# Kernel tuning notes

Measured on AMD Instinct MI355X. Metric: run time of the kernel, lower is better.

The kernel has to match this reference:

```python
import jax, jax.numpy as jnp
import numpy as np

N = 50000
E = 800000
IN = 64
HID = 64
OUT = 32
R = 8
B = 8
EPS = 1e-5


def setup_inputs() -> dict:
    key = jax.random.key(0)
    ks = jax.random.split(key, 20)
    s_in = 1.0 / np.sqrt(IN)
    s_hid = 1.0 / np.sqrt(HID)
    inp = {
        "x": jax.random.normal(ks[0], (N, IN), dtype=jnp.float32),
        "edge_index": jax.random.randint(ks[1], (2, E), 0, N, dtype=jnp.int64) if jax.config.jax_enable_x64 else jax.random.randint(ks[1], (2, E), 0, N),
        "edge_type": jax.random.randint(ks[2], (E,), 0, R),
        # conv1: in -> hid
        "comp1": jax.random.normal(ks[3], (R, B), dtype=jnp.float32) * (1.0 / np.sqrt(B)),
        "bases1": jax.random.normal(ks[4], (B, IN, HID), dtype=jnp.float32) * s_in,
        "root1": jax.random.normal(ks[5], (IN, HID), dtype=jnp.float32) * s_in,
        "bias1": jnp.zeros((HID,), dtype=jnp.float32),
        # conv2 (hidden): hid -> hid
        "comp2": jax.random.normal(ks[6], (R, B), dtype=jnp.float32) * (1.0 / np.sqrt(B)),
        "bases2": jax.random.normal(ks[7], (B, HID, HID), dtype=jnp.float32) * s_hid,
        "root2": jax.random.normal(ks[8], (HID, HID), dtype=jnp.float32) * s_hid,
        "bias2": jnp.zeros((HID,), dtype=jnp.float32),
        # conv_out: hid -> out
        "comp3": jax.random.normal(ks[9], (R, B), dtype=jnp.float32) * (1.0 / np.sqrt(B)),
        "bases3": jax.random.normal(ks[10], (B, HID, OUT), dtype=jnp.float32) * s_hid,
        "root3": jax.random.normal(ks[11], (HID, OUT), dtype=jnp.float32) * s_hid,
        "bias3": jnp.zeros((OUT,), dtype=jnp.float32),
        # batchnorms
        "gamma1": jnp.ones((HID,), dtype=jnp.float32),
        "beta1": jnp.zeros((HID,), dtype=jnp.float32),
        "gamma2": jnp.ones((HID,), dtype=jnp.float32),
        "beta2": jnp.zeros((HID,), dtype=jnp.float32),
    }
    return inp


def rgcn_conv(x, src, dst, etype, comp, bases, root, bias):
    """PyG-style RGCNConv with basis decomposition and per-relation mean aggregation."""
    n = x.shape[0]
    # project node features through all bases: [N, B, O]
    xb = jnp.einsum('ni,bio->nbo', x, bases)
    # per-edge relation coefficients [E, B] contract with gathered basis features [E, B, O]
    msg = jnp.einsum('eb,ebo->eo', comp[etype], xb[src])
    # mean normalization per (dst node, relation)
    seg = dst * R + etype
    cnt = jax.ops.segment_sum(jnp.ones((msg.shape[0],), dtype=x.dtype), seg, num_segments=n * R)
    msg = msg / jnp.maximum(cnt[seg], 1.0)[:, None]
    agg = jax.ops.segment_sum(msg, dst, num_segments=n)
    return agg + x @ root + bias


def batch_norm(x, gamma, beta):
    mu = jnp.mean(x, axis=0)
    var = jnp.mean(jnp.square(x - mu), axis=0)  # biased, as torch BN training
    return (x - mu) * jax.lax.rsqrt(var + EPS) * gamma + beta


def reference(x, edge_index, edge_type, comp1, bases1, root1, bias1,
              comp2, bases2, root2, bias2, comp3, bases3, root3, bias3,
              gamma1, beta1, gamma2, beta2):
    src, dst = edge_index[0], edge_index[1]
    h = rgcn_conv(x, src, dst, edge_type, comp1, bases1, root1, bias1)
    h = batch_norm(jax.nn.relu(h), gamma1, beta1)  # dropout = identity (eval)
    h_res = h  # residual since in_channels == hidden_channels
    h2 = rgcn_conv(h, src, dst, edge_type, comp2, bases2, root2, bias2)
    h2 = batch_norm(jax.nn.relu(h2), gamma2, beta2)
    h = h2 + h_res
    out = rgcn_conv(h, src, dst, edge_type, comp3, bases3, root3, bias3)
    return out
```

## Files before the change

### kernel.cpp

```cpp
#include <hip/hip_runtime.h>

#define NN 50000
#define NE 800000
#define RR 8
#define BB 8
#define EPSV 1e-5f
#define SCAN_B ((NN + 255) / 256)
#define NGRP 64

typedef unsigned short bfu;
typedef signed char i8;
typedef __attribute__((ext_vector_type(8))) short bf16x8;
typedef __attribute__((ext_vector_type(4))) float f32x4;

__device__ inline float bf2f(bfu u) { return __uint_as_float(((unsigned)u) << 16); }
__device__ inline bfu f2bf(float f) {
    unsigned u = __float_as_uint(f);
    return (bfu)((u + 0x7fffu + ((u >> 16) & 1u)) >> 16);
}

#define NW1 36864L
#define NW2 36864L
#define NW3 18432L
#define NZ  (400000L + 50000L + 2L * NGRP * 128)

__device__ inline void build_one(const float* __restrict__ comp, const float* __restrict__ bases,
                                 const float* __restrict__ root, bfu* __restrict__ Wp,
                                 int O, int idx) {
    int k = idx / O, o = idx % O;
    float val;
    if (k < 512) {
        int r = k >> 6, i = k & 63;
        val = 0.f;
#pragma unroll
        for (int b = 0; b < BB; ++b)
            val += comp[r * BB + b] * bases[(b * 64 + i) * O + o];
    } else {
        val = root[(k - 512) * O + o];
    }
    int kt = k >> 5, kk = k & 31;
    int lane = ((kk >> 3) << 4) | (o & 15);
    int pos = ((kt * (O / 16) + (o >> 4)) * 64 + lane) * 8 + (kk & 7);
    Wp[pos] = f2bf(val);
}

__global__ void prep(const float* __restrict__ c1, const float* __restrict__ b1,
                     const float* __restrict__ r1, bfu* __restrict__ Wp1,
                     const float* __restrict__ c2, const float* __restrict__ b2,
                     const float* __restrict__ r2, bfu* __restrict__ Wp2,
                     const float* __restrict__ c3, const float* __restrict__ b3,
                     const float* __restrict__ r3, bfu* __restrict__ Wp3,
                     float* __restrict__ zbase) {
    long i = (long)blockIdx.x * blockDim.x + threadIdx.x;
    long stride = (long)gridDim.x * blockDim.x;
    const long tot = NW1 + NW2 + NW3 + NZ;
    for (; i < tot; i += stride) {
        if (i < NW1) build_one(c1, b1, r1, Wp1, 64, (int)i);
        else if (i < NW1 + NW2) build_one(c2, b2, r2, Wp2, 64, (int)(i - NW1));
        else if (i < NW1 + NW2 + NW3) build_one(c3, b3, r3, Wp3, 32, (int)(i - NW1 - NW2));
        else zbase[i - (NW1 + NW2 + NW3)] = 0.f;
    }
}

__global__ __launch_bounds__(256) void cvt_rows(const float* __restrict__ x,
                                                bfu* __restrict__ xb,
                                                i8* __restrict__ x8,
                                                float* __restrict__ xs) {
    int wv = threadIdx.x >> 6, lane = threadIdx.x & 63;
    int gw = blockIdx.x * 4 + wv, nw = gridDim.x * 4;
    for (int n = gw; n < NN; n += nw) {
        float v = x[(size_t)n * 64 + lane];
        xb[(size_t)n * 64 + lane] = f2bf(v);
        float am = fabsf(v);
#pragma unroll
        for (int d = 1; d < 64; d <<= 1) am = fmaxf(am, __shfl_xor(am, d));
        am = fmaxf(am, 1e-20f);
        float inv = 127.f / am;
        x8[(size_t)n * 64 + lane] = (i8)__float2int_rn(v * inv);
        if (lane == 0) xs[n] = am * (1.f / 127.f);
    }
}

__global__ void edge_count(const int* __restrict__ ei, const int* __restrict__ et,
                           float* __restrict__ cnt) {
    int range = blockIdx.x >> 8;
    int lo = range * (NN / 8), hi = lo + NN / 8;
    int i = (blockIdx.x & 255) * 256 + threadIdx.x;
    for (int e = i; e < NE; e += 256 * 256) {
        int d = ei[NE + e];
        if (d >= lo && d < hi)
            atomicAdd(&cnt[(size_t)d * RR + et[e]], 1.0f);
    }
}

__global__ void scan1(const float* __restrict__ cnt, int* __restrict__ offs, int* __restrict__ bsum) {
    __shared__ int sh[256];
    int b = blockIdx.x, t = threadIdx.x;
    int i = b * 256 + t;
    int v = 0;
    if (i < NN) {
        float s = 0.f;
#pragma unroll
        for (int r = 0; r < RR; ++r) s += cnt[(size_t)i * RR + r];
        v = (int)s;
    }
    sh[t] = v;
    __syncthreads();
    for (int s = 1; s < 256; s <<= 1) {
        int tmp = (t >= s) ? sh[t - s] : 0;
        __syncthreads();
        sh[t] += tmp;
        __syncthreads();
    }
    if (i < NN) offs[i] = sh[t] - v;
    if (t == 255) bsum[b] = sh[255];
}

__global__ void scan2(int* __restrict__ bsum, int* __restrict__ offs) {
    if (threadIdx.x == 0 && blockIdx.x == 0) {
        int run = 0;
        for (int b = 0; b < SCAN_B; ++b) { int t = bsum[b]; bsum[b] = run; run += t; }
        offs[NN] = run;
    }
}

__global__ void scan3(int* __restrict__ offs, const int* __restrict__ bsum) {
    int b = blockIdx.x, t = threadIdx.x;
    int i = b * 256 + t;
    if (i < NN) offs[i] += bsum[b];
}

__global__ void place(const int* __restrict__ ei, const int* __restrict__ et,
                      const int* __restrict__ offs, int* __restrict__ fill,
                      unsigned* __restrict__ esrt) {
    int range = blockIdx.x >> 8;
    int lo = range * (NN / 8), hi = lo + NN / 8;
    int i = (blockIdx.x & 255) * 256 + threadIdx.x;
    for (int e = i; e < NE; e += 256 * 256) {
        int d = ei[NE + e];
        if (d >= lo && d < hi) {
            int pos = offs[d] + atomicAdd(&fill[d], 1);
            esrt[pos] = ((unsigned)ei[e] << 3) | (unsigned)et[e];
        }
    }
}

#define ACCUMS(SU, V)                          \
    switch ((SU) & 7) {                        \
        case 0: a0 += (V); break;              \
        case 1: a1 += (V); break;              \
        case 2: a2 += (V); break;              \
        case 3: a3 += (V); break;              \
        case 4: a4 += (V); break;              \
        case 5: a5 += (V); break;              \
        case 6: a6 += (V); break;              \
        default: a7 += (V); break;             \
    }
#define RDL(X, L) __builtin_amdgcn_readlane((int)(X), (L))

template <int O, bool RELU, bool STATS>
__global__ __launch_bounds__(512, 8) void agg_gemm(const int* __restrict__ offs,
                                                   const unsigned* __restrict__ esrt,
                                                   const float* __restrict__ cnt,
                                                   const i8* __restrict__ x8,
                                                   const float* __restrict__ xs,
                                                   const bfu* __restrict__ xb,
                                                   const bfu* __restrict__ Wp,
                                                   const float* __restrict__ bias,
                                                   float* __restrict__ outp,
                                                   float* __restrict__ stats) {
    constexpr int CT = O / 16;
    __shared__ bfu Af[1152 * 8];
    int wave = threadIdx.x >> 6, lane = threadIdx.x & 63;
    int n0 = blockIdx.x * 16;
    int c = lane;
    int swz_lo = ((c >> 3) & 3) << 4;

#pragma unroll 1
    for (int i = 0; i < 2; ++i) {
        int row = wave * 2 + i;
        int n = n0 + row;
        int j0 = offs[n], j1 = offs[n + 1];
        float a0 = 0.f, a1 = 0.f, a2 = 0.f, a3 = 0.f, a4 = 0.f, a5 = 0.f, a6 = 0.f, a7 = 0.f;
        int j = j0;
        for (; j + 8 <= j1; j += 8) {
            unsigned mye = esrt[j + (lane & 7)];
            int s0 = RDL(mye, 0), s1 = RDL(mye, 1), s2 = RDL(mye, 2), s3 = RDL(mye, 3);
            int s4 = RDL(mye, 4), s5 = RDL(mye, 5), s6 = RDL(mye, 6), s7 = RDL(mye, 7);
            float q0 = (float)x8[(size_t)((unsigned)s0 >> 3) * 64 + lane];
            float q1 = (float)x8[(size_t)((unsigned)s1 >> 3) * 64 + lane];
            float q2 = (float)x8[(size_t)((unsigned)s2 >> 3) * 64 + lane];
            float q3 = (float)x8[(size_t)((unsigned)s3 >> 3) * 64 + lane];
            float q4 = (float)x8[(size_t)((unsigned)s4 >> 3) * 64 + lane];
            float q5 = (float)x8[(size_t)((unsigned)s5 >> 3) * 64 + lane];
            float q6 = (float)x8[(size_t)((unsigned)s6 >> 3) * 64 + lane];
            float q7 = (float)x8[(size_t)((unsigned)s7 >> 3) * 64 + lane];
            float c0 = xs[(unsigned)s0 >> 3], c1 = xs[(unsigned)s1 >> 3];
            float c2 = xs[(unsigned)s2 >> 3], c3 = xs[(unsigned)s3 >> 3];
            float c4 = xs[(unsigned)s4 >> 3], c5 = xs[(unsigned)s5 >> 3];
            float c6 = xs[(unsigned)s6 >> 3], c7 = xs[(unsigned)s7 >> 3];
            ACCUMS(s0, q0 * c0) ACCUMS(s1, q1 * c1) ACCUMS(s2, q2 * c2) ACCUMS(s3, q3 * c3)
            ACCUMS(s4, q4 * c4) ACCUMS(s5, q5 * c5) ACCUMS(s6, q6 * c6) ACCUMS(s7, q7 * c7)
        }
        if (j + 4 <= j1) {
            unsigned mye = esrt[j + (lane & 3)];
            int s0 = RDL(mye, 0), s1 = RDL(mye, 1), s2 = RDL(mye, 2), s3 = RDL(mye, 3);
            float q0 = (float)x8[(size_t)((unsigned)s0 >> 3) * 64 + lane];
            float q1 = (float)x8[(size_t)((unsigned)s1 >> 3) * 64 + lane];
            float q2 = (float)x8[(size_t)((unsigned)s2 >> 3) * 64 + lane];
            float q3 = (float)x8[(size_t)((unsigned)s3 >> 3) * 64 + lane];
            float c0 = xs[(unsigned)s0 >> 3], c1 = xs[(unsigned)s1 >> 3];
            float c2 = xs[(unsigned)s2 >> 3], c3 = xs[(unsigned)s3 >> 3];
            ACCUMS(s0, q0 * c0) ACCUMS(s1, q1 * c1) ACCUMS(s2, q2 * c2) ACCUMS(s3, q3 * c3)
            j += 4;
        }
        for (; j < j1; ++j) {
            int s0 = __builtin_amdgcn_readfirstlane((int)esrt[j]);
            float q0 = (float)x8[(size_t)((unsigned)s0 >> 3) * 64 + lane];
            float c0 = xs[(unsigned)s0 >> 3];
            ACCUMS(s0, q0 * c0)
        }
#define WR(r, ar) {                                                            \
        float inv = 1.f / fmaxf(cnt[(size_t)n * RR + (r)], 1.f);               \
        bfu bv = f2bf((ar) * inv);                                             \
        int g = (2 * (r) + (c >> 5)) * 64 + (row | swz_lo);                    \
        int gs = g ^ ((g >> 3) & 7) ^ ((g >> 6) & 7);                          \
        Af[gs * 8 + (c & 7)] = bv; }
        WR(0, a0) WR(1, a1) WR(2, a2) WR(3, a3)
        WR(4, a4) WR(5, a5) WR(6, a6) WR(7, a7)
#undef WR
        {
            bfu bv = xb[(size_t)n * 64 + lane];
            int g = (16 + (c >> 5)) * 64 + (row | swz_lo);
            int gs = g ^ ((g >> 3) & 7) ^ ((g >> 6) & 7);
            Af[gs * 8 + (c & 7)] = bv;
        }
    }
    __syncthreads();

    int ct = wave;
    if (ct < CT) {
        f32x4 acc = (f32x4){0.f, 0.f, 0.f, 0.f};
#pragma unroll
        for (int kt = 0; kt < 18; ++kt) {
            int g = kt * 64 + lane;
            int gs = g ^ ((g >> 3) & 7) ^ ((g >> 6) & 7);
            bf16x8 af = *(const bf16x8*)&Af[gs * 8];
            bf16x8 bfv = *(const bf16x8*)&Wp[((size_t)(kt * CT + ct) * 64 + lane) * 8];
            acc = __builtin_amdgcn_mfma_f32_16x16x32_bf16(af, bfv, acc, 0, 0, 0);
        }
        int col = ct * 16 + (lane & 15);
        float b = bias[col];
        float ssum = 0.f, sq = 0.f;
#pragma unroll
        for (int jj = 0; jj < 4; ++jj) {
            int row = (lane >> 4) * 4 + jj;
            float v = acc[jj] + b;
            if (RELU) v = fmaxf(v, 0.f);
            outp[(size_t)(n0 + row) * O + col] = v;
            if (STATS) { ssum += v; sq += v * v; }
        }
        if (STATS) {
            ssum += __shfl_xor(ssum, 16); ssum += __shfl_xor(ssum, 32);
            sq   += __shfl_xor(sq, 16);   sq   += __shfl_xor(sq, 32);
            if ((lane >> 4) == 0) {
                int g = blockIdx.x & (NGRP - 1);
                atomicAdd(&stats[g * 128 + col], ssum);
                atomicAdd(&stats[g * 128 + 64 + col], sq);
            }
        }
    }
}

template <bool HASRES>
__global__ __launch_bounds__(256) void bn_apply(const float* __restrict__ y,
                                                const float* __restrict__ stats,
                                                const float* __restrict__ gamma,
                                                const float* __restrict__ beta,
                                                const bfu* __restrict__ resb,
                                                bfu* __restrict__ hb,
                                                i8* __restrict__ h8,
                                                float* __restrict__ hs) {
    __shared__ float sc[128];
    int t = threadIdx.x;
    if (t < 64) {
        float s = 0.f, q = 0.f;
        for (int g = 0; g < NGRP; ++g) {
            s += stats[g * 128 + t];
            q += stats[g * 128 + 64 + t];
        }
        float mu = s / (float)NN;
        float var = q / (float)NN - mu * mu;
        float scale = gamma[t] * rsqrtf(var + EPSV);
        sc[t] = scale;
        sc[64 + t] = beta[t] - mu * scale;
    }
    __syncthreads();
    int wv = threadIdx.x >> 6, lane = threadIdx.x & 63;
    int gw = blockIdx.x * 4 + wv, nw = gridDim.x * 4;
    for (int n = gw; n < NN; n += nw) {
        float v = y[(size_t)n * 64 + lane] * sc[lane] + sc[64 + lane];
        if (HASRES) v += bf2f(resb[(size_t)n * 64 + lane]);
        hb[(size_t)n * 64 + lane] = f2bf(v);
        float am = fabsf(v);
#pragma unroll
        for (int d = 1; d < 64; d <<= 1) am = fmaxf(am, __shfl_xor(am, d));
        am = fmaxf(am, 1e-20f);
        float inv = 127.f / am;
        h8[(size_t)n * 64 + lane] = (i8)__float2int_rn(v * inv);
        if (lane == 0) hs[n] = am * (1.f / 127.f);
    }
}

extern "C" void kernel_launch(void* const* d_in, const int* in_sizes, int n_in,
                              void* d_out, int out_size, void* d_ws, size_t ws_size,
                              hipStream_t stream) {
    const float* x      = (const float*)d_in[0];
    const int*   ei     = (const int*)d_in[1];
    const int*   et     = (const int*)d_in[2];
    const float* comp1  = (const float*)d_in[3];
    const float* bases1 = (const float*)d_in[4];
    const float* root1  = (const float*)d_in[5];
    const float* bias1  = (const float*)d_in[6];
    const float* comp2  = (const float*)d_in[7];
    const float* bases2 = (const float*)d_in[8];
    const float* root2  = (const float*)d_in[9];
    const float* bias2  = (const float*)d_in[10];
    const float* comp3  = (const float*)d_in[11];
    const float* bases3 = (const float*)d_in[12];
    const float* root3  = (const float*)d_in[13];
    const float* bias3  = (const float*)d_in[14];
    const float* gamma1 = (const float*)d_in[15];
    const float* beta1  = (const float*)d_in[16];
    const float* gamma2 = (const float*)d_in[17];
    const float* beta2  = (const float*)d_in[18];
    float* out = (float*)d_out;

    float* ws = (float*)d_ws;
    size_t off = 0;
    bfu* Wp1 = (bfu*)(ws + off); off += 18432;
    bfu* Wp2 = (bfu*)(ws + off); off += 18432;
    bfu* Wp3 = (bfu*)(ws + off); off += 9216;
    float* cnt    = ws + off; off += (size_t)NN * RR;
    int*   fill   = (int*)(ws + off); off += NN;
    float* stats1 = ws + off; off += NGRP * 128;
    float* stats2 = ws + off; off += NGRP * 128;
    float* y  = ws + off; off += (size_t)NN * 64;
    bfu* xb   = (bfu*)(ws + off); off += (size_t)NN * 32;
    bfu* h1b  = (bfu*)(ws + off); off += (size_t)NN * 32;
    bfu* hb   = (bfu*)(ws + off); off += (size_t)NN * 32;
    i8*  x8   = (i8*)(ws + off);  off += (size_t)NN * 16;
    i8*  h1_8 = (i8*)(ws + off);  off += (size_t)NN * 16;
    i8*  h_8  = (i8*)(ws + off);  off += (size_t)NN * 16;
    float* xsc  = ws + off; off += NN;
    float* h1sc = ws + off; off += NN;
    float* hsc  = ws + off; off += NN;
    int* offs = (int*)(ws + off); off += NN + 4;
    int* bsum = (int*)(ws + off); off += 256;
    unsigned* esrt = (unsigned*)(ws + off); off += NE;

    prep<<<dim3(1024), dim3(256), 0, stream>>>(comp1, bases1, root1, Wp1,
                                               comp2, bases2, root2, Wp2,
                                               comp3, bases3, root3, Wp3, cnt);
    cvt_rows<<<dim3(512), dim3(256), 0, stream>>>(x, xb, x8, xsc);
    edge_count<<<dim3(2048), dim3(256), 0, stream>>>(ei, et, cnt);
    scan1<<<dim3(SCAN_B), dim3(256), 0, stream>>>(cnt, offs, bsum);
    scan2<<<dim3(1), dim3(64), 0, stream>>>(bsum, offs);
    scan3<<<dim3(SCAN_B), dim3(256), 0, stream>>>(offs, bsum);
    place<<<dim3(2048), dim3(256), 0, stream>>>(ei, et, offs, fill, esrt);

    agg_gemm<64, true, true><<<dim3(NN / 16), dim3(512), 0, stream>>>(offs, esrt, cnt, x8, xsc, xb, Wp1, bias1, y, stats1);
    bn_apply<false><<<dim3(1024), dim3(256), 0, stream>>>(y, stats1, gamma1, beta1, nullptr, h1b, h1_8, h1sc);

    agg_gemm<64, true, true><<<dim3(NN / 16), dim3(512), 0, stream>>>(offs, esrt, cnt, h1_8, h1sc, h1b, Wp2, bias2, y, stats2);
    bn_apply<true><<<dim3(1024), dim3(256), 0, stream>>>(y, stats2, gamma2, beta2, h1b, hb, h_8, hsc);

    agg_gemm<32, false, false><<<dim3(NN / 16), dim3(512), 0, stream>>>(offs, esrt, cnt, h_8, hsc, hb, Wp3, bias3, out, nullptr);
}
```

Baseline: 304.9 us.

## Use one row per wave, prefetch edge batches, and broadcast scales via readlane

agg_gemm now runs 16 waves per block, each handling one destination row instead of two in sequence, which exposes more parallel gather latency. The edge index batch for the next iteration is prefetched, and per-source scales are loaded once per lane and broadcast with readlane instead of eight scalar loads. edge_count and place now split the destination range into 4 partitions instead of 8, which halves their grids. The larger 1024-thread blocks may reduce occupancy flexibility, and with fewer partitions the atomics are less localized.

```diff
diff --git a/kernel.cpp b/kernel.cpp
--- a/kernel.cpp
+++ b/kernel.cpp
@@ -84,7 +84,7 @@
 __global__ void edge_count(const int* __restrict__ ei, const int* __restrict__ et,
                            float* __restrict__ cnt) {
     int range = blockIdx.x >> 8;
-    int lo = range * (NN / 8), hi = lo + NN / 8;
+    int lo = range * (NN / 4), hi = lo + NN / 4;
     int i = (blockIdx.x & 255) * 256 + threadIdx.x;
     for (int e = i; e < NE; e += 256 * 256) {
         int d = ei[NE + e];
@@ -134,7 +134,7 @@
                       const int* __restrict__ offs, int* __restrict__ fill,
                       unsigned* __restrict__ esrt) {
     int range = blockIdx.x >> 8;
-    int lo = range * (NN / 8), hi = lo + NN / 8;
+    int lo = range * (NN / 4), hi = lo + NN / 4;
     int i = (blockIdx.x & 255) * 256 + threadIdx.x;
     for (int e = i; e < NE; e += 256 * 256) {
         int d = ei[NE + e];
@@ -159,82 +159,88 @@
 #define RDL(X, L) __builtin_amdgcn_readlane((int)(X), (L))
 
 template <int O, bool RELU, bool STATS>
-__global__ __launch_bounds__(512, 8) void agg_gemm(const int* __restrict__ offs,
-                                                   const unsigned* __restrict__ esrt,
-                                                   const float* __restrict__ cnt,
-                                                   const i8* __restrict__ x8,
-                                                   const float* __restrict__ xs,
-                                                   const bfu* __restrict__ xb,
-                                                   const bfu* __restrict__ Wp,
-                                                   const float* __restrict__ bias,
-                                                   float* __restrict__ outp,
-                                                   float* __restrict__ stats) {
+__global__ __launch_bounds__(1024, 8) void agg_gemm(const int* __restrict__ offs,
+                                                    const unsigned* __restrict__ esrt,
+                                                    const float* __restrict__ cnt,
+                                                    const i8* __restrict__ x8,
+                                                    const float* __restrict__ xs,
+                                                    const bfu* __restrict__ xb,
+                                                    const bfu* __restrict__ Wp,
+                                                    const float* __restrict__ bias,
+                                                    float* __restrict__ outp,
+                                                    float* __restrict__ stats) {
     constexpr int CT = O / 16;
     __shared__ bfu Af[1152 * 8];
     int wave = threadIdx.x >> 6, lane = threadIdx.x & 63;
     int n0 = blockIdx.x * 16;
+    int row = wave;
+    int n = n0 + row;
     int c = lane;
     int swz_lo = ((c >> 3) & 3) << 4;
 
-#pragma unroll 1
-    for (int i = 0; i < 2; ++i) {
-        int row = wave * 2 + i;
-        int n = n0 + row;
-        int j0 = offs[n], j1 = offs[n + 1];
-        float a0 = 0.f, a1 = 0.f, a2 = 0.f, a3 = 0.f, a4 = 0.f, a5 = 0.f, a6 = 0.f, a7 = 0.f;
-        int j = j0;
-        for (; j + 8 <= j1; j += 8) {
-            unsigned mye = esrt[j + (lane & 7)];
-            int s0 = RDL(mye, 0), s1 = RDL(mye, 1), s2 = RDL(mye, 2), s3 = RDL(mye, 3);
-            int s4 = RDL(mye, 4), s5 = RDL(mye, 5), s6 = RDL(mye, 6), s7 = RDL(mye, 7);
-            float q0 = (float)x8[(size_t)((unsigned)s0 >> 3) * 64 + lane];
-            float q1 = (float)x8[(size_t)((unsigned)s1 >> 3) * 64 + lane];
-            float q2 = (float)x8[(size_t)((unsigned)s2 >> 3) * 64 + lane];
-            float q3 = (float)x8[(size_t)((unsigned)s3 >> 3) * 64 + lane];
-            float q4 = (float)x8[(size_t)((unsigned)s4 >> 3) * 64 + lane];
-            float q5 = (float)x8[(size_t)((unsigned)s5 >> 3) * 64 + lane];
-            float q6 = (float)x8[(size_t)((unsigned)s6 >> 3) * 64 + lane];
-            float q7 = (float)x8[(size_t)((unsigned)s7 >> 3) * 64 + lane];
-            float c0 = xs[(unsigned)s0 >> 3], c1 = xs[(unsigned)s1 >> 3];
-            float c2 = xs[(unsigned)s2 >> 3], c3 = xs[(unsigned)s3 >> 3];
-            float c4 = xs[(unsigned)s4 >> 3], c5 = xs[(unsigned)s5 >> 3];
-            float c6 = xs[(unsigned)s6 >> 3], c7 = xs[(unsigned)s7 >> 3];
-            ACCUMS(s0, q0 * c0) ACCUMS(s1, q1 * c1) ACCUMS(s2, q2 * c2) ACCUMS(s3, q3 * c3)
-            ACCUMS(s4, q4 * c4) ACCUMS(s5, q5 * c5) ACCUMS(s6, q6 * c6) ACCUMS(s7, q7 * c7)
-        }
-        if (j + 4 <= j1) {
-            unsigned mye = esrt[j + (lane & 3)];
-            int s0 = RDL(mye, 0), s1 = RDL(mye, 1), s2 = RDL(mye, 2), s3 = RDL(mye, 3);
-            float q0 = (float)x8[(size_t)((unsigned)s0 >> 3) * 64 + lane];
-            float q1 = (float)x8[(size_t)((unsigned)s1 >> 3) * 64 + lane];
-            float q2 = (float)x8[(size_t)((unsigned)s2 >> 3) * 64 + lane];
-            float q3 = (float)x8[(size_t)((unsigned)s3 >> 3) * 64 + lane];
-            float c0 = xs[(unsigned)s0 >> 3], c1 = xs[(unsigned)s1 >> 3];
-            float c2 = xs[(unsigned)s2 >> 3], c3 = xs[(unsigned)s3 >> 3];
-            ACCUMS(s0, q0 * c0) ACCUMS(s1, q1 * c1) ACCUMS(s2, q2 * c2) ACCUMS(s3, q3 * c3)
-            j += 4;
-        }
-        for (; j < j1; ++j) {
-            int s0 = __builtin_amdgcn_readfirstlane((int)esrt[j]);
-            float q0 = (float)x8[(size_t)((unsigned)s0 >> 3) * 64 + lane];
-            float c0 = xs[(unsigned)s0 >> 3];
-            ACCUMS(s0, q0 * c0)
-        }
+    int j0 = offs[n], j1 = offs[n + 1];
+    float a0 = 0.f, a1 = 0.f, a2 = 0.f, a3 = 0.f, a4 = 0.f, a5 = 0.f, a6 = 0.f, a7 = 0.f;
+    int j = j0;
+    unsigned mye = 0;
+    if (j + 8 <= j1) mye = esrt[j + (lane & 7)];
+    for (; j + 8 <= j1;) {
+        unsigned cur = mye;
+        float sc8 = xs[cur >> 3];
+        int jn = j + 8;
+        if (jn + 8 <= j1) mye = esrt[jn + (lane & 7)];
+        int scb = __float_as_int(sc8);
+        int s0 = RDL(cur, 0), s1 = RDL(cur, 1), s2 = RDL(cur, 2), s3 = RDL(cur, 3);
+        int s4 = RDL(cur, 4), s5 = RDL(cur, 5), s6 = RDL(cur, 6), s7 = RDL(cur, 7);
+        float q0 = (float)x8[(size_t)((unsigned)s0 >> 3) * 64 + lane];
+        float q1 = (float)x8[(size_t)((unsigned)s1 >> 3) * 64 + lane];
+        float q2 = (float)x8[(size_t)((unsigned)s2 >> 3) * 64 + lane];
+        float q3 = (float)x8[(size_t)((unsigned)s3 >> 3) * 64 + lane];
+        float q4 = (float)x8[(size_t)((unsigned)s4 >> 3) * 64 + lane];
+        float q5 = (float)x8[(size_t)((unsigned)s5 >> 3) * 64 + lane];
+        float q6 = (float)x8[(size_t)((unsigned)s6 >> 3) * 64 + lane];
+        float q7 = (float)x8[(size_t)((unsigned)s7 >> 3) * 64 + lane];
+        float c0 = __int_as_float(RDL(scb, 0)), c1 = __int_as_float(RDL(scb, 1));
+        float c2 = __int_as_float(RDL(scb, 2)), c3 = __int_as_float(RDL(scb, 3));
+        float c4 = __int_as_float(RDL(scb, 4)), c5 = __int_as_float(RDL(scb, 5));
+        float c6 = __int_as_float(RDL(scb, 6)), c7 = __int_as_float(RDL(scb, 7));
+        ACCUMS(s0, q0 * c0) ACCUMS(s1, q1 * c1) ACCUMS(s2, q2 * c2) ACCUMS(s3, q3 * c3)
+        ACCUMS(s4, q4 * c4) ACCUMS(s5, q5 * c5) ACCUMS(s6, q6 * c6) ACCUMS(s7, q7 * c7)
+        j = jn;
+    }
+    if (j + 4 <= j1) {
+        unsigned m4 = esrt[j + (lane & 3)];
+        float sc4 = xs[m4 >> 3];
+        int scb = __float_as_int(sc4);
+        int s0 = RDL(m4, 0), s1 = RDL(m4, 1), s2 = RDL(m4, 2), s3 = RDL(m4, 3);
+        float q0 = (float)x8[(size_t)((unsigned)s0 >> 3) * 64 + lane];
+        float q1 = (float)x8[(size_t)((unsigned)s1 >> 3) * 64 + lane];
+        float q2 = (float)x8[(size_t)((unsigned)s2 >> 3) * 64 + lane];
+        float q3 = (float)x8[(size_t)((unsigned)s3 >> 3) * 64 + lane];
+        float c0 = __int_as_float(RDL(scb, 0)), c1 = __int_as_float(RDL(scb, 1));
+        float c2 = __int_as_float(RDL(scb, 2)), c3 = __int_as_float(RDL(scb, 3));
+        ACCUMS(s0, q0 * c0) ACCUMS(s1, q1 * c1) ACCUMS(s2, q2 * c2) ACCUMS(s3, q3 * c3)
+        j += 4;
+    }
+    for (; j < j1; ++j) {
+        int s0 = __builtin_amdgcn_readfirstlane((int)esrt[j]);
+        float q0 = (float)x8[(size_t)((unsigned)s0 >> 3) * 64 + lane];
+        float c0 = xs[(unsigned)s0 >> 3];
+        ACCUMS(s0, q0 * c0)
+    }
 #define WR(r, ar) {                                                            \
-        float inv = 1.f / fmaxf(cnt[(size_t)n * RR + (r)], 1.f);               \
-        bfu bv = f2bf((ar) * inv);                                             \
-        int g = (2 * (r) + (c >> 5)) * 64 + (row | swz_lo);                    \
-        int gs = g ^ ((g >> 3) & 7) ^ ((g >> 6) & 7);                          \
-        Af[gs * 8 + (c & 7)] = bv; }
-        WR(0, a0) WR(1, a1) WR(2, a2) WR(3, a3)
-        WR(4, a4) WR(5, a5) WR(6, a6) WR(7, a7)
+    float inv = 1.f / fmaxf(cnt[(size_t)n * RR + (r)], 1.f);                   \
+    bfu bv = f2bf((ar) * inv);                                                 \
+    int g = (2 * (r) + (c >> 5)) * 64 + (row | swz_lo);                        \
+    int gs = g ^ ((g >> 3) & 7) ^ ((g >> 6) & 7);                              \
+    Af[gs * 8 + (c & 7)] = bv; }
+    WR(0, a0) WR(1, a1) WR(2, a2) WR(3, a3)
+    WR(4, a4) WR(5, a5) WR(6, a6) WR(7, a7)
 #undef WR
-        {
-            bfu bv = xb[(size_t)n * 64 + lane];
-            int g = (16 + (c >> 5)) * 64 + (row | swz_lo);
-            int gs = g ^ ((g >> 3) & 7) ^ ((g >> 6) & 7);
-            Af[gs * 8 + (c & 7)] = bv;
-        }
+    {
+        bfu bv = xb[(size_t)n * 64 + lane];
+        int g = (16 + (c >> 5)) * 64 + (row | swz_lo);
+        int gs = g ^ ((g >> 3) & 7) ^ ((g >> 6) & 7);
+        Af[gs * 8 + (c & 7)] = bv;
     }
     __syncthreads();
 
@@ -254,10 +260,10 @@
         float ssum = 0.f, sq = 0.f;
 #pragma unroll
         for (int jj = 0; jj < 4; ++jj) {
-            int row = (lane >> 4) * 4 + jj;
+            int orow = (lane >> 4) * 4 + jj;
             float v = acc[jj] + b;
             if (RELU) v = fmaxf(v, 0.f);
-            outp[(size_t)(n0 + row) * O + col] = v;
+            outp[(size_t)(n0 + orow) * O + col] = v;
             if (STATS) { ssum += v; sq += v * v; }
         }
         if (STATS) {
@@ -363,17 +369,17 @@
                                                comp2, bases2, root2, Wp2,
                                                comp3, bases3, root3, Wp3, cnt);
     cvt_rows<<<dim3(512), dim3(256), 0, stream>>>(x, xb, x8, xsc);
-    edge_count<<<dim3(2048), dim3(256), 0, stream>>>(ei, et, cnt);
+    edge_count<<<dim3(1024), dim3(256), 0, stream>>>(ei, et, cnt);
     scan1<<<dim3(SCAN_B), dim3(256), 0, stream>>>(cnt, offs, bsum);
     scan2<<<dim3(1), dim3(64), 0, stream>>>(bsum, offs);
     scan3<<<dim3(SCAN_B), dim3(256), 0, stream>>>(offs, bsum);
-    place<<<dim3(2048), dim3(256), 0, stream>>>(ei, et, offs, fill, esrt);
-
-    agg_gemm<64, true, true><<<dim3(NN / 16), dim3(512), 0, stream>>>(offs, esrt, cnt, x8, xsc, xb, Wp1, bias1, y, stats1);
+    place<<<dim3(1024), dim3(256), 0, stream>>>(ei, et, offs, fill, esrt);
+
+    agg_gemm<64, true, true><<<dim3(NN / 16), dim3(1024), 0, stream>>>(offs, esrt, cnt, x8, xsc, xb, Wp1, bias1, y, stats1);
     bn_apply<false><<<dim3(1024), dim3(256), 0, stream>>>(y, stats1, gamma1, beta1, nullptr, h1b, h1_8, h1sc);
 
-    agg_gemm<64, true, true><<<dim3(NN / 16), dim3(512), 0, stream>>>(offs, esrt, cnt, h1_8, h1sc, h1b, Wp2, bias2, y, stats2);
+    agg_gemm<64, true, true><<<dim3(NN / 16), dim3(1024), 0, stream>>>(offs, esrt, cnt, h1_8, h1sc, h1b, Wp2, bias2, y, stats2);
     bn_apply<true><<<dim3(1024), dim3(256), 0, stream>>>(y, stats2, gamma2, beta2, h1b, hb, h_8, hsc);
 
-    agg_gemm<32, false, false><<<dim3(NN / 16), dim3(512), 0, stream>>>(offs, esrt, cnt, h_8, hsc, hb, Wp3, bias3, out, nullptr);
-}
+    agg_gemm<32, false, false><<<dim3(NN / 16), dim3(1024), 0, stream>>>(offs, esrt, cnt, h_8, hsc, hb, Wp3, bias3, out, nullptr);
+}
```

Measured after the change: 313.8 us. 2.9% more time.
